# Kernel tuning notes

Hardware: AMD Instinct MI355X
Metric: run time of the kernel (lower is better)

Reference implementation:

```python
import jax, jax.numpy as jnp
import numpy as np

B, N, D, H = 4, 2048, 1024, 16
HD = D // H
SCALE = HD ** -0.5

def neg_softmax(x):
    # sign(x) * softmax(|x|) along last axis
    return jnp.sign(x) * jax.nn.softmax(jnp.abs(x), axis=-1)

def setup_inputs() -> dict:
    key = jax.random.key(0)
    ks = jax.random.split(key, 9)
    s = 0.02
    return {
        "x": jax.random.normal(ks[0], (B, N, D), jnp.float32),
        "Wq": jax.random.normal(ks[1], (D, D), jnp.float32) * s,
        "bq": jax.random.normal(ks[2], (D,), jnp.float32) * s,
        "Wk": jax.random.normal(ks[3], (D, D), jnp.float32) * s,
        "bk": jax.random.normal(ks[4], (D,), jnp.float32) * s,
        "Wv": jax.random.normal(ks[5], (D, D), jnp.float32) * s,
        "bv": jax.random.normal(ks[6], (D,), jnp.float32) * s,
        "Wo": jax.random.normal(ks[7], (D, D), jnp.float32) * s,
        "bo": jax.random.normal(ks[8], (D,), jnp.float32) * s,
    }

def reference(x, Wq, bq, Wk, bk, Wv, bv, Wo, bo):
    def heads(t):  # [B,N,D] -> [B,H,N,hd]
        return t.reshape(B, N, H, HD).transpose(0, 2, 1, 3)
    Q = heads(x @ Wq.T + bq)
    K = heads(x @ Wk.T + bk)
    V = heads(x @ Wv.T + bv)
    logits = jnp.einsum('bhnd,bhmd->bhnm', Q, K) * SCALE
    attn = neg_softmax(logits)
    out = jnp.einsum('bhnm,bhmd->bhnd', attn, V)
    out = out.transpose(0, 2, 1, 3).reshape(B, N, D)
    return out @ Wo.T + bo
```

## Files before the change

### kernel.cpp

```cpp
#include <hip/hip_runtime.h>

typedef _Float16 f16x8 __attribute__((ext_vector_type(8)));
typedef __fp16 h16x2 __attribute__((ext_vector_type(2)));
typedef float f32x4 __attribute__((ext_vector_type(4)));
typedef unsigned short u16x4 __attribute__((ext_vector_type(4)));

#define NB 4
#define NSEQ 2048
#define NH 16
#define HDIM 64
#define DM 1024
#define MROWS (NB * NSEQ)

#define AS1 __attribute__((address_space(1)))
#define AS3 __attribute__((address_space(3)))

__device__ __forceinline__ float exp2_fast(float x) {
  float r; asm("v_exp_f32 %0, %1" : "=v"(r) : "v"(x)); return r;
}

__device__ __forceinline__ unsigned short f2h(float f) {
  _Float16 h = (_Float16)f;
  union { _Float16 h; unsigned short u; } v; v.h = h;
  return v.u;
}

__global__ void cvt_kernel(const float* __restrict__ in, unsigned short* __restrict__ out, int n4) {
  int i = blockIdx.x * blockDim.x + threadIdx.x;
  if (i < n4) {
    const float4 v = ((const float4*)in)[i];
    u16x4 o;
    o.x = f2h(v.x); o.y = f2h(v.y); o.z = f2h(v.z); o.w = f2h(v.w);
    ((u16x4*)out)[i] = o;
  }
}

__global__ void cvt4_kernel(const float* __restrict__ w0, const float* __restrict__ w1,
                            const float* __restrict__ w2, const float* __restrict__ w3,
                            unsigned short* __restrict__ o0, unsigned short* __restrict__ o1,
                            unsigned short* __restrict__ o2, unsigned short* __restrict__ o3) {
  const int i = blockIdx.x * blockDim.x + threadIdx.x;
  const float* src; unsigned short* dst;
  switch (blockIdx.y) {
    case 0: src = w0; dst = o0; break;
    case 1: src = w1; dst = o1; break;
    case 2: src = w2; dst = o2; break;
    default: src = w3; dst = o3; break;
  }
  const float4 v = ((const float4*)src)[i];
  u16x4 o;
  o.x = f2h(v.x); o.y = f2h(v.y); o.z = f2h(v.z); o.w = f2h(v.w);
  ((u16x4*)dst)[i] = o;
}

template<int OUT_F16>
__global__ __launch_bounds__(256)
void gemm_bt(const unsigned short* __restrict__ A, const unsigned short* __restrict__ Bw,
             const float* __restrict__ bias, void* __restrict__ Cv, float scale) {
  __shared__ unsigned short As[128 * 32];
  __shared__ unsigned short Bs[128 * 32];
  const int tid = threadIdx.x, lane = tid & 63, wave = tid >> 6;
  const int g = lane >> 4, c = lane & 15;
  const int orig = blockIdx.y * 8 + blockIdx.x;
  const int wg = (orig & 7) * 64 + (orig >> 3);
  const int m0 = (wg >> 3) * 128, n0 = (wg & 7) * 128;
  const int wm = (wave >> 1) * 64, wn = (wave & 1) * 64;
  f32x4 acc[4][4] = {};
  for (int kt = 0; kt < 1024; kt += 32) {
#pragma unroll
    for (int p = 0; p < 2; ++p) {
      const int idx = p * 256 + tid;
      const int row = idx >> 2, col = (idx & 3) * 8;
      __builtin_amdgcn_global_load_lds(
          (const AS1 void*)(A + (size_t)(m0 + row) * 1024 + kt + col),
          (AS3 void*)(As + idx * 8), 16, 0, 0);
      __builtin_amdgcn_global_load_lds(
          (const AS1 void*)(Bw + (size_t)(n0 + row) * 1024 + kt + col),
          (AS3 void*)(Bs + idx * 8), 16, 0, 0);
    }
    __syncthreads();
    f16x8 af[4], bfr[4];
#pragma unroll
    for (int i = 0; i < 4; ++i) af[i] = *(const f16x8*)(As + (wm + i * 16 + c) * 32 + g * 8);
#pragma unroll
    for (int i = 0; i < 4; ++i) bfr[i] = *(const f16x8*)(Bs + (wn + i * 16 + c) * 32 + g * 8);
#pragma unroll
    for (int i = 0; i < 4; ++i)
#pragma unroll
      for (int j = 0; j < 4; ++j)
        acc[i][j] = __builtin_amdgcn_mfma_f32_16x16x32_f16(af[i], bfr[j], acc[i][j], 0, 0, 0);
    __syncthreads();
  }
#pragma unroll
  for (int i = 0; i < 4; ++i)
#pragma unroll
    for (int j = 0; j < 4; ++j)
#pragma unroll
      for (int r = 0; r < 4; ++r) {
        const int row = m0 + wm + i * 16 + g * 4 + r;
        const int col = n0 + wn + j * 16 + c;
        const float v = (acc[i][j][r] + bias[col]) * scale;
        if (OUT_F16) ((unsigned short*)Cv)[(size_t)row * 1024 + col] = f2h(v);
        else         ((float*)Cv)[(size_t)row * 1024 + col] = v;
      }
}

__global__ __launch_bounds__(256, 2)
void attn_kernel(const unsigned short* __restrict__ Qg, const unsigned short* __restrict__ Kg,
                 const unsigned short* __restrict__ Vg, unsigned short* __restrict__ Og) {
  __shared__ __align__(16) unsigned short Kl[2][64 * 64];
  __shared__ __align__(16) unsigned short Vt[2][64 * 72];
  const int tid = threadIdx.x, lane = tid & 63, wave = tid >> 6;
  const int g = lane >> 4, c = lane & 15;
  const int orig = blockIdx.y * 8 + blockIdx.x;
  const int wg = (orig & 7) * 64 + (orig >> 3);
  const int qblk = wg & 7, bh = wg >> 3;
  const int b = bh >> 4, h = bh & 15;
  const int q0 = qblk * 256 + wave * 64;
  const size_t rb = (size_t)b * NSEQ;
  const int hc = h * HDIM;
  const int NT = NSEQ / 64;

  const int k_kvo = tid >> 3;
  const int k_d   = (((tid & 7) ^ ((tid >> 3) & 7)) * 8);
  const int v_kv = lane;
  const int pv = (v_kv & 32) | (((v_kv >> 2) & 3) << 3) | (((v_kv >> 4) & 1) << 2) | (v_kv & 3);

  f16x8 qf[4][2];
#pragma unroll
  for (int m = 0; m < 4; ++m)
#pragma unroll
    for (int kb2 = 0; kb2 < 2; ++kb2)
      qf[m][kb2] = *(const f16x8*)(Qg + (rb + q0 + m * 16 + c) * DM + hc + kb2 * 32 + g * 8);

  f32x4 oT[4][4] = {};
  float dpart[4] = {0.f, 0.f, 0.f, 0.f};
  f16x8 vreg[2];

  auto stageK = [&](int t, int buf) {
    const int kv0 = t * 64;
#pragma unroll
    for (int p = 0; p < 2; ++p) {
      const int kv = kv0 + 32 * p + k_kvo;
      __builtin_amdgcn_global_load_lds(
          (const AS1 void*)(Kg + (rb + kv) * DM + hc + k_d),
          (AS3 void*)(&Kl[buf][p * 2048 + tid * 8]), 16, 0, 0);
    }
  };
  auto loadV = [&](int t) {
    const int kv0 = t * 64;
#pragma unroll
    for (int p = 0; p < 2; ++p)
      vreg[p] = *(const f16x8*)(Vg + (rb + kv0 + v_kv) * DM + hc + p * 32 + wave * 8);
  };
  auto writeV = [&](int buf) {
#pragma unroll
    for (int p = 0; p < 2; ++p) {
      const int vd = p * 32 + wave * 8;
      union { f16x8 v; unsigned short u[8]; } vv; vv.v = vreg[p];
#pragma unroll
      for (int j = 0; j < 8; ++j) Vt[buf][(vd + j) * 72 + pv] = vv.u[j];
    }
  };

  stageK(0, 0);
  loadV(0);
  writeV(0);
  __syncthreads();

  for (int t = 0; t < NT; ++t) {
    const int cur = t & 1;
    if (t + 1 < NT) { stageK(t + 1, cur ^ 1); loadV(t + 1); }

    const unsigned short* KL = Kl[cur];
    const unsigned short* VT = Vt[cur];

    f16x8 kf[2][4];
#pragma unroll
    for (int kb2 = 0; kb2 < 2; ++kb2)
#pragma unroll
      for (int nb = 0; nb < 4; ++nb)
        kf[kb2][nb] = *(const f16x8*)(KL + (nb * 16 + c) * 64 + (((kb2 * 32 + g * 8) ^ ((c & 7) * 8))));
    f16x8 vtf[2][4];
#pragma unroll
    for (int kb2 = 0; kb2 < 2; ++kb2)
#pragma unroll
      for (int db = 0; db < 4; ++db)
        vtf[kb2][db] = *(const f16x8*)(VT + (db * 16 + c) * 72 + kb2 * 32 + g * 8);

#pragma unroll
    for (int m = 0; m < 4; ++m) {
      f32x4 s[4] = {};
#pragma unroll
      for (int nb = 0; nb < 4; ++nb)
#pragma unroll
        for (int kb2 = 0; kb2 < 2; ++kb2)
          s[nb] = __builtin_amdgcn_mfma_f32_16x16x32_f16(kf[kb2][nb], qf[m][kb2], s[nb], 0, 0, 0);

      union PW { f16x8 v; h16x2 w[4]; } pf[2];
      float es0 = 0.f, es1 = 0.f;
#pragma unroll
      for (int nb = 0; nb < 4; ++nb) {
        float p[4];
#pragma unroll
        for (int r = 0; r < 4; ++r) {
          const float sv = s[nb][r];
          const float e = exp2_fast(fabsf(sv) - 18.0f);
          if (r & 1) es1 += e; else es0 += e;
          p[r] = copysignf(e, sv);
        }
        pf[nb >> 1].w[(nb & 1) * 2]     = __builtin_amdgcn_cvt_pkrtz(p[0], p[1]);
        pf[nb >> 1].w[(nb & 1) * 2 + 1] = __builtin_amdgcn_cvt_pkrtz(p[2], p[3]);
      }
      dpart[m] += es0 + es1;

#pragma unroll
      for (int db = 0; db < 4; ++db) {
        oT[db][m] = __builtin_amdgcn_mfma_f32_16x16x32_f16(vtf[0][db], pf[0].v, oT[db][m], 0, 0, 0);
        oT[db][m] = __builtin_amdgcn_mfma_f32_16x16x32_f16(vtf[1][db], pf[1].v, oT[db][m], 0, 0, 0);
      }
    }

    if (t + 1 < NT) writeV(cur ^ 1);
    __syncthreads();
  }

#pragma unroll
  for (int m = 0; m < 4; ++m) {
    float d = dpart[m];
    d += __shfl_xor(d, 16);
    d += __shfl_xor(d, 32);
    const float inv = 1.f / d;
#pragma unroll
    for (int db = 0; db < 4; ++db) {
      h16x2 h01 = __builtin_amdgcn_cvt_pkrtz(oT[db][m][0] * inv, oT[db][m][1] * inv);
      h16x2 h23 = __builtin_amdgcn_cvt_pkrtz(oT[db][m][2] * inv, oT[db][m][3] * inv);
      union { h16x2 h; unsigned u; } a, bb; a.h = h01; bb.h = h23;
      union { uint2 u2; unsigned u[2]; } st;
      st.u[0] = a.u; st.u[1] = bb.u;
      *(uint2*)(Og + (rb + q0 + m * 16 + c) * DM + hc + db * 16 + g * 4) = st.u2;
    }
  }
}

extern "C" void kernel_launch(void* const* d_in, const int* in_sizes, int n_in,
                              void* d_out, int out_size, void* d_ws, size_t ws_size,
                              hipStream_t stream) {
  const float* x  = (const float*)d_in[0];
  const float* Wq = (const float*)d_in[1];
  const float* bq = (const float*)d_in[2];
  const float* Wk = (const float*)d_in[3];
  const float* bk = (const float*)d_in[4];
  const float* Wv = (const float*)d_in[5];
  const float* bv = (const float*)d_in[6];
  const float* Wo = (const float*)d_in[7];
  const float* bo = (const float*)d_in[8];
  float* out = (float*)d_out;

  unsigned short* xb  = (unsigned short*)d_ws;
  unsigned short* wqb = xb  + (size_t)MROWS * DM;
  unsigned short* wkb = wqb + (size_t)DM * DM;
  unsigned short* wvb = wkb + (size_t)DM * DM;
  unsigned short* wob = wvb + (size_t)DM * DM;
  unsigned short* qb  = wob + (size_t)DM * DM;
  unsigned short* kb  = qb  + (size_t)MROWS * DM;
  unsigned short* vb  = kb  + (size_t)MROWS * DM;
  unsigned short* ab  = xb;

  cvt_kernel<<<(MROWS * DM) / 1024, 256, 0, stream>>>(x, xb, (MROWS * DM) / 4);
  cvt4_kernel<<<dim3((DM * DM) / 1024, 4), 256, 0, stream>>>(Wq, Wk, Wv, Wo, wqb, wkb, wvb, wob);

  const dim3 gg(DM / 128, MROWS / 128);
  const float SC = 0.125f * 1.4426950408889634f;
  gemm_bt<1><<<gg, 256, 0, stream>>>(xb, wqb, bq, qb, SC);
  gemm_bt<1><<<gg, 256, 0, stream>>>(xb, wkb, bk, kb, 1.f);
  gemm_bt<1><<<gg, 256, 0, stream>>>(xb, wvb, bv, vb, 1.f);

  attn_kernel<<<dim3(NSEQ / 256, NB * NH), 256, 0, stream>>>(qb, kb, vb, ab);

  gemm_bt<0><<<gg, 256, 0, stream>>>(ab, wob, bo, out, 1.f);
}
```

Baseline: 205.8 us.

## Reload Q fragments per tile to raise attention occupancy, fuse conversion kernels

The attention kernel no longer keeps the Q fragments in registers for the whole loop. It reloads them from global memory (L1/L2) on every KV tile, which frees VGPRs so launch bounds can rise from 2 to 3 blocks per CU. MFMA sections are wrapped in s_setprio so waves in the matrix phase get issue priority. The two fp32-to-fp16 conversion kernels are merged into one launch. The cost is repeated Q reads on each tile, adding memory traffic and latency inside the inner loop.

```diff
diff --git a/kernel.cpp b/kernel.cpp
--- a/kernel.cpp
+++ b/kernel.cpp
@@ -25,27 +25,24 @@
   return v.u;
 }
 
-__global__ void cvt_kernel(const float* __restrict__ in, unsigned short* __restrict__ out, int n4) {
-  int i = blockIdx.x * blockDim.x + threadIdx.x;
-  if (i < n4) {
-    const float4 v = ((const float4*)in)[i];
-    u16x4 o;
-    o.x = f2h(v.x); o.y = f2h(v.y); o.z = f2h(v.z); o.w = f2h(v.w);
-    ((u16x4*)out)[i] = o;
-  }
-}
-
-__global__ void cvt4_kernel(const float* __restrict__ w0, const float* __restrict__ w1,
-                            const float* __restrict__ w2, const float* __restrict__ w3,
-                            unsigned short* __restrict__ o0, unsigned short* __restrict__ o1,
-                            unsigned short* __restrict__ o2, unsigned short* __restrict__ o3) {
-  const int i = blockIdx.x * blockDim.x + threadIdx.x;
-  const float* src; unsigned short* dst;
-  switch (blockIdx.y) {
-    case 0: src = w0; dst = o0; break;
-    case 1: src = w1; dst = o1; break;
-    case 2: src = w2; dst = o2; break;
-    default: src = w3; dst = o3; break;
+__global__ void cvt_all_kernel(const float* __restrict__ x, const float* __restrict__ w0,
+                               const float* __restrict__ w1, const float* __restrict__ w2,
+                               const float* __restrict__ w3, unsigned short* __restrict__ xo,
+                               unsigned short* __restrict__ o0, unsigned short* __restrict__ o1,
+                               unsigned short* __restrict__ o2, unsigned short* __restrict__ o3) {
+  const int id = blockIdx.x * blockDim.x + threadIdx.x;
+  const float* src; unsigned short* dst; int i;
+  if (id < (MROWS * DM) / 4) { src = x; dst = xo; i = id; }
+  else {
+    const int id2 = id - (MROWS * DM) / 4;
+    const int w = id2 >> 18;
+    i = id2 & 262143;
+    switch (w) {
+      case 0: src = w0; dst = o0; break;
+      case 1: src = w1; dst = o1; break;
+      case 2: src = w2; dst = o2; break;
+      default: src = w3; dst = o3; break;
+    }
   }
   const float4 v = ((const float4*)src)[i];
   u16x4 o;
@@ -105,7 +102,7 @@
       }
 }
 
-__global__ __launch_bounds__(256, 2)
+__global__ __launch_bounds__(256, 3)
 void attn_kernel(const unsigned short* __restrict__ Qg, const unsigned short* __restrict__ Kg,
                  const unsigned short* __restrict__ Vg, unsigned short* __restrict__ Og) {
   __shared__ __align__(16) unsigned short Kl[2][64 * 64];
@@ -126,12 +123,7 @@
   const int v_kv = lane;
   const int pv = (v_kv & 32) | (((v_kv >> 2) & 3) << 3) | (((v_kv >> 4) & 1) << 2) | (v_kv & 3);
 
-  f16x8 qf[4][2];
-#pragma unroll
-  for (int m = 0; m < 4; ++m)
-#pragma unroll
-    for (int kb2 = 0; kb2 < 2; ++kb2)
-      qf[m][kb2] = *(const f16x8*)(Qg + (rb + q0 + m * 16 + c) * DM + hc + kb2 * 32 + g * 8);
+  const unsigned short* qbase = Qg + (rb + q0 + c) * DM + hc + g * 8;
 
   f32x4 oT[4][4] = {};
   float dpart[4] = {0.f, 0.f, 0.f, 0.f};
@@ -175,6 +167,9 @@
     const unsigned short* KL = Kl[cur];
     const unsigned short* VT = Vt[cur];
 
+    const unsigned short* Qt = qbase;
+    asm volatile("" : "+v"(Qt));
+
     f16x8 kf[2][4];
 #pragma unroll
     for (int kb2 = 0; kb2 < 2; ++kb2)
@@ -190,12 +185,19 @@
 
 #pragma unroll
     for (int m = 0; m < 4; ++m) {
+      f16x8 qm[2];
+#pragma unroll
+      for (int kb2 = 0; kb2 < 2; ++kb2)
+        qm[kb2] = *(const f16x8*)(Qt + m * 16 * DM + kb2 * 32);
+
       f32x4 s[4] = {};
+      __builtin_amdgcn_s_setprio(1);
 #pragma unroll
       for (int nb = 0; nb < 4; ++nb)
 #pragma unroll
         for (int kb2 = 0; kb2 < 2; ++kb2)
-          s[nb] = __builtin_amdgcn_mfma_f32_16x16x32_f16(kf[kb2][nb], qf[m][kb2], s[nb], 0, 0, 0);
+          s[nb] = __builtin_amdgcn_mfma_f32_16x16x32_f16(kf[kb2][nb], qm[kb2], s[nb], 0, 0, 0);
+      __builtin_amdgcn_s_setprio(0);
 
       union PW { f16x8 v; h16x2 w[4]; } pf[2];
       float es0 = 0.f, es1 = 0.f;
@@ -214,11 +216,13 @@
       }
       dpart[m] += es0 + es1;
 
+      __builtin_amdgcn_s_setprio(1);
 #pragma unroll
       for (int db = 0; db < 4; ++db) {
         oT[db][m] = __builtin_amdgcn_mfma_f32_16x16x32_f16(vtf[0][db], pf[0].v, oT[db][m], 0, 0, 0);
         oT[db][m] = __builtin_amdgcn_mfma_f32_16x16x32_f16(vtf[1][db], pf[1].v, oT[db][m], 0, 0, 0);
       }
+      __builtin_amdgcn_s_setprio(0);
     }
 
     if (t + 1 < NT) writeV(cur ^ 1);
@@ -267,8 +271,8 @@
   unsigned short* vb  = kb  + (size_t)MROWS * DM;
   unsigned short* ab  = xb;
 
-  cvt_kernel<<<(MROWS * DM) / 1024, 256, 0, stream>>>(x, xb, (MROWS * DM) / 4);
-  cvt4_kernel<<<dim3((DM * DM) / 1024, 4), 256, 0, stream>>>(Wq, Wk, Wv, Wo, wqb, wkb, wvb, wob);
+  cvt_all_kernel<<<(MROWS * DM / 4 + 4 * DM * DM / 4) / 256, 256, 0, stream>>>(
+      x, Wq, Wk, Wv, Wo, xb, wqb, wkb, wvb, wob);
 
   const dim3 gg(DM / 128, MROWS / 128);
   const float SC = 0.125f * 1.4426950408889634f;
```

New measurement: 390.6 us. +89.8%, slower.
